# Performance work log

Measured on AMD Instinct MI355X. Metric: run time of the kernel, lower is better.

Reference implementation:

```python
import jax, jax.numpy as jnp
import numpy as np

N_NODES = 50000
N_EDGES = 600000
D_FEAT = 128
NHID = 128
N_CLASSES = 40


def gcn_conv(x, W, b, src, dst, n_nodes):
    """PyG-style GCNConv: out = D^{-1/2} (A + I) D^{-1/2} (x W) + b.

    src/dst: [E'] edge endpoints including self-loops; messages are gathered
    from src and scatter-added at dst with symmetric normalization.
    """
    h = x @ W  # [N, out] -- transform before propagate (linearity => same math)
    deg = jax.ops.segment_sum(jnp.ones_like(dst, dtype=h.dtype), dst,
                              num_segments=n_nodes)  # in-degree incl. self-loop
    dinv = jnp.where(deg > 0, jax.lax.rsqrt(deg), 0.0)
    norm = dinv[src] * dinv[dst]  # [E']
    msg = h[src] * norm[:, None]  # [E', out] gather + scale
    out = jax.ops.segment_sum(msg, dst, num_segments=n_nodes)  # scatter-add
    return out + b


def setup_inputs() -> dict:
    key = jax.random.key(0)
    ks = jax.random.split(key, 8)
    x = jax.random.normal(ks[0], (N_NODES, D_FEAT), dtype=jnp.float32)
    edge_index = jax.random.randint(ks[1], (2, N_EDGES), 0, N_NODES, dtype=jnp.int64)
    # Glorot-ish scaled params
    W1 = jax.random.normal(ks[2], (D_FEAT, NHID), dtype=jnp.float32) / np.sqrt(D_FEAT)
    b1 = jnp.zeros((NHID,), dtype=jnp.float32)
    W2 = jax.random.normal(ks[3], (NHID, NHID), dtype=jnp.float32) / np.sqrt(NHID)
    b2 = jnp.zeros((NHID,), dtype=jnp.float32)
    Wlin = jax.random.normal(ks[4], (NHID, N_CLASSES), dtype=jnp.float32) / np.sqrt(NHID)
    blin = jnp.zeros((N_CLASSES,), dtype=jnp.float32)
    return {"x": x, "edge_index": edge_index, "W1": W1, "b1": b1,
            "W2": W2, "b2": b2, "Wlin": Wlin, "blin": blin}


def reference(x, edge_index, W1, b1, W2, b2, Wlin, blin):
    n = x.shape[0]
    loop = jnp.arange(n, dtype=edge_index.dtype)
    src = jnp.concatenate([edge_index[0], loop])  # add self-loops
    dst = jnp.concatenate([edge_index[1], loop])
    h = gcn_conv(x, W1, b1, src, dst, n)
    h = jnp.tanh(h)  # dropout is identity in eval mode
    h = gcn_conv(h, W2, b2, src, dst, n)
    h = jnp.tanh(h)
    return h @ Wlin + blin  # [N, num_classes]
```

## Files before the change

### kernel.cpp

```cpp
#include <hip/hip_runtime.h>
#include <cmath>

#define D 128
#define NCLS 40
#define GG 391
#define CAP 64

typedef __bf16 bfrag __attribute__((ext_vector_type(8)));
typedef float ffrag __attribute__((ext_vector_type(4)));
typedef unsigned int u32;
typedef unsigned int u32x4 __attribute__((ext_vector_type(4)));

__device__ inline float fast_tanh(float x) {
  float ax = __builtin_fabsf(x);
  float z = __expf(-2.0f * ax);
  float r = (1.0f - z) * __builtin_amdgcn_rcpf(1.0f + z);
  return copysignf(r, x);
}

__global__ __launch_bounds__(256) void zero_deg(int* __restrict__ deg, int N) {
  int i = blockIdx.x * 256 + threadIdx.x;
  if (i < N) deg[i] = 0;
}

__global__ __launch_bounds__(256) void mega1(const float* __restrict__ A, const float* __restrict__ W1,
                                             const float* __restrict__ W2, const float* __restrict__ Wl,
                                             __bf16* __restrict__ C, int N,
                                             const int* __restrict__ src, const int* __restrict__ dst, int E,
                                             int* __restrict__ deg, int* __restrict__ csr,
                                             __bf16* __restrict__ Wt2, __bf16* __restrict__ Wlt, int EB) {
  const int b = blockIdx.x;
  const int tid = threadIdx.x;
  if (b >= GG) {
    if (b < GG + EB) {
      int e = (b - GG) * 256 + tid;
      if (e < E) {
        int s = src[e], d = dst[e];
        int pos = atomicAdd(&deg[d], 1);
        if (pos < CAP) csr[d * CAP + pos] = s;
      }
    } else {
      int j = (b - GG - EB) * 256 + tid;
      if (j < 16384) {
        Wt2[j] = (__bf16)W2[(j & 127) * D + (j >> 7)];
      } else if (j < 16384 + 48 * D) {
        int q = j - 16384;
        int n = q >> 7, k = q & 127;
        Wlt[q] = (n < NCLS) ? (__bf16)Wl[k * NCLS + n] : (__bf16)0.0f;
      }
    }
    return;
  }
  __shared__ __align__(16) __bf16 Bs[128][136];
  const int wave = tid >> 6, lane = tid & 63;
  const int row0 = b * 128 + wave * 32;
  const int koff = (lane >> 4) * 8;

  for (int i = tid; i < 128 * 128; i += 256) {
    int n = i & 127, k = i >> 7;
    Bs[n][k] = (__bf16)W1[k * D + n];
  }

  bfrag a[2][4];
#pragma unroll
  for (int mt = 0; mt < 2; ++mt) {
    int r = row0 + mt * 16 + (lane & 15);
    int rc = r < N ? r : N - 1;
    const float* p = A + (size_t)rc * D;
#pragma unroll
    for (int kk = 0; kk < 4; ++kk) {
      float4 u = *(const float4*)(p + kk * 32 + koff);
      float4 v = *(const float4*)(p + kk * 32 + koff + 4);
      bfrag f;
      f[0] = (__bf16)u.x; f[1] = (__bf16)u.y; f[2] = (__bf16)u.z; f[3] = (__bf16)u.w;
      f[4] = (__bf16)v.x; f[5] = (__bf16)v.y; f[6] = (__bf16)v.z; f[7] = (__bf16)v.w;
      a[mt][kk] = f;
    }
  }
  __syncthreads();

  ffrag acc[2][8];
#pragma unroll
  for (int mt = 0; mt < 2; ++mt)
#pragma unroll
    for (int n = 0; n < 8; ++n) acc[mt][n] = (ffrag){0.f, 0.f, 0.f, 0.f};

#pragma unroll
  for (int kk = 0; kk < 4; ++kk) {
#pragma unroll
    for (int n = 0; n < 8; ++n) {
      bfrag bb = *(const bfrag*)(&Bs[n * 16 + (lane & 15)][kk * 32 + koff]);
      acc[0][n] = __builtin_amdgcn_mfma_f32_16x16x32_bf16(a[0][kk], bb, acc[0][n], 0, 0, 0);
      acc[1][n] = __builtin_amdgcn_mfma_f32_16x16x32_bf16(a[1][kk], bb, acc[1][n], 0, 0, 0);
    }
  }

  int ocol = lane & 15;
#pragma unroll
  for (int mt = 0; mt < 2; ++mt) {
    int orow0 = row0 + mt * 16 + (lane >> 4) * 4;
#pragma unroll
    for (int n = 0; n < 8; ++n)
#pragma unroll
      for (int i = 0; i < 4; ++i) {
        int r = orow0 + i;
        if (r < N) C[(size_t)r * D + n * 16 + ocol] = (__bf16)acc[mt][n][i];
      }
  }
}

__device__ inline void gather16(const __bf16* __restrict__ t, const int* __restrict__ deg,
                                const int* __restrict__ csr, const float* __restrict__ bias,
                                __bf16 (*Hs)[136], int node0, int wave, int lane, int N) {
  const int g = lane >> 4, sl = lane & 15;
  const int node = node0 + wave * 4 + g;
  const int nd = node < N ? node : N - 1;
  const int cnt = deg[nd];
  const int jm = cnt < CAP ? cnt : CAP;
  const float dv = rsqrtf((float)cnt + 1.0f);

  int mx = jm;
  int o1 = __shfl_xor(mx, 16, 64);
  mx = mx > o1 ? mx : o1;
  int o2 = __shfl_xor(mx, 32, 64);
  mx = mx > o2 ? mx : o2;
  const int jmw = __builtin_amdgcn_readfirstlane(mx);

  bfrag tv = *(const bfrag*)(t + (size_t)nd * D + sl * 8);
  const float selfw = dv * dv;
  float acc[8];
#pragma unroll
  for (int i = 0; i < 8; ++i) acc[i] = selfw * (float)tv[i];

  for (int base = 0; base < jmw; base += 16) {
    int rem = jm - base;
    int es = nd;
    float ew = 0.0f;
    if (sl < rem) {
      es = csr[nd * CAP + base + sl];
      ew = rsqrtf((float)deg[es] + 1.0f) * dv;
    }
    int nin = jmw - base; nin = nin < 16 ? nin : 16;
    for (int j = 0; j < nin; ++j) {
      int s = __shfl(es, g * 16 + j, 64);
      float w = __shfl(ew, g * 16 + j, 64);
      bfrag r = *(const bfrag*)(t + (size_t)s * D + sl * 8);
#pragma unroll
      for (int i = 0; i < 8; ++i) acc[i] += w * (float)r[i];
    }
  }

  float4 b0 = *(const float4*)(bias + sl * 8);
  float4 b1 = *(const float4*)(bias + sl * 8 + 4);
  bfrag o;
  o[0] = (__bf16)fast_tanh(acc[0] + b0.x);
  o[1] = (__bf16)fast_tanh(acc[1] + b0.y);
  o[2] = (__bf16)fast_tanh(acc[2] + b0.z);
  o[3] = (__bf16)fast_tanh(acc[3] + b0.w);
  o[4] = (__bf16)fast_tanh(acc[4] + b1.x);
  o[5] = (__bf16)fast_tanh(acc[5] + b1.y);
  o[6] = (__bf16)fast_tanh(acc[6] + b1.z);
  o[7] = (__bf16)fast_tanh(acc[7] + b1.w);
  *(u32x4*)&Hs[wave * 4 + g][sl * 8] = *(u32x4*)&o;
}

__global__ __launch_bounds__(256) void gather_gemm(const __bf16* __restrict__ t, const int* __restrict__ deg,
                                                   const int* __restrict__ csr, const float* __restrict__ bias,
                                                   const __bf16* __restrict__ Wt, __bf16* __restrict__ C, int N) {
  __shared__ __align__(16) __bf16 Hs[16][136];
  const int tid = threadIdx.x;
  const int wave = tid >> 6, lane = tid & 63;
  const int g = lane >> 4, sl = lane & 15;
  const int node0 = blockIdx.x * 16;

  gather16(t, deg, csr, bias, Hs, node0, wave, lane, N);
  __syncthreads();

  const int koff = g * 8;
  bfrag a[4];
#pragma unroll
  for (int kk = 0; kk < 4; ++kk) a[kk] = *(const bfrag*)(&Hs[sl][kk * 32 + koff]);
  ffrag acc2[2];
  acc2[0] = (ffrag){0.f, 0.f, 0.f, 0.f};
  acc2[1] = (ffrag){0.f, 0.f, 0.f, 0.f};
#pragma unroll
  for (int nt = 0; nt < 2; ++nt) {
    const __bf16* wp = Wt + (size_t)(wave * 32 + nt * 16 + sl) * D;
    bfrag bfr[4];
#pragma unroll
    for (int kk = 0; kk < 4; ++kk) bfr[kk] = *(const bfrag*)(wp + kk * 32 + koff);
#pragma unroll
    for (int kk = 0; kk < 4; ++kk)
      acc2[nt] = __builtin_amdgcn_mfma_f32_16x16x32_bf16(a[kk], bfr[kk], acc2[nt], 0, 0, 0);
  }
#pragma unroll
  for (int nt = 0; nt < 2; ++nt) {
    int ccol = wave * 32 + nt * 16 + sl;
#pragma unroll
    for (int i = 0; i < 4; ++i) {
      int r = node0 + g * 4 + i;
      if (r < N) C[(size_t)r * D + ccol] = (__bf16)acc2[nt][i];
    }
  }
}

__global__ __launch_bounds__(256) void gather_head(const __bf16* __restrict__ t, const int* __restrict__ deg,
                                                   const int* __restrict__ csr, const float* __restrict__ bias,
                                                   const __bf16* __restrict__ Wlt, const float* __restrict__ blin,
                                                   float* __restrict__ out, int N) {
  __shared__ __align__(16) __bf16 Hs[16][136];
  const int tid = threadIdx.x;
  const int wave = tid >> 6, lane = tid & 63;
  const int g = lane >> 4, sl = lane & 15;
  const int node0 = blockIdx.x * 16;

  gather16(t, deg, csr, bias, Hs, node0, wave, lane, N);
  __syncthreads();

  if (wave < 3) {
    const int koff = g * 8;
    bfrag a[4];
#pragma unroll
    for (int kk = 0; kk < 4; ++kk) a[kk] = *(const bfrag*)(&Hs[sl][kk * 32 + koff]);
    ffrag acc2 = (ffrag){0.f, 0.f, 0.f, 0.f};
    const __bf16* wp = Wlt + (size_t)(wave * 16 + sl) * D;
    bfrag bfr[4];
#pragma unroll
    for (int kk = 0; kk < 4; ++kk) bfr[kk] = *(const bfrag*)(wp + kk * 32 + koff);
#pragma unroll
    for (int kk = 0; kk < 4; ++kk)
      acc2 = __builtin_amdgcn_mfma_f32_16x16x32_bf16(a[kk], bfr[kk], acc2, 0, 0, 0);

    int ccol = wave * 16 + sl;
    if (ccol < NCLS) {
      float bl = blin[ccol];
#pragma unroll
      for (int i = 0; i < 4; ++i) {
        int r = node0 + g * 4 + i;
        if (r < N) out[(size_t)r * NCLS + ccol] = acc2[i] + bl;
      }
    }
  }
}

extern "C" void kernel_launch(void* const* d_in, const int* in_sizes, int n_in,
                              void* d_out, int out_size, void* d_ws, size_t ws_size,
                              hipStream_t stream) {
  const float* x    = (const float*)d_in[0];
  const int*   ei   = (const int*)d_in[1];
  const float* W1   = (const float*)d_in[2];
  const float* b1   = (const float*)d_in[3];
  const float* W2   = (const float*)d_in[4];
  const float* b2   = (const float*)d_in[5];
  const float* Wlin = (const float*)d_in[6];
  const float* blin = (const float*)d_in[7];
  float* out = (float*)d_out;

  const int N = in_sizes[0] / D;
  const int E = in_sizes[1] / 2;
  const int* srcp = ei;
  const int* dstp = ei + E;

  char* ws = (char*)d_ws;
  int*    deg = (int*)ws;
  __bf16* Wt2 = (__bf16*)(ws + ((size_t)256 << 10));
  __bf16* Wlt = (__bf16*)(ws + ((size_t)320 << 10));
  int*    csr = (int*)(ws + ((size_t)1 << 20));
  __bf16* tb  = (__bf16*)(ws + ((size_t)16 << 20));
  __bf16* hb  = (__bf16*)(ws + ((size_t)32 << 20));

  const int nb = (N + 255) / 256;
  const int eb = (E + 255) / 256;
  const int cvb = (16384 + 48 * D + 255) / 256;
  const int gb = (N + 15) / 16;
  dim3 b256(256);

  zero_deg<<<nb, b256, 0, stream>>>(deg, N);
  mega1<<<GG + eb + cvb, b256, 0, stream>>>(x, W1, W2, Wlin, tb, N, srcp, dstp, E, deg, csr, Wt2, Wlt, eb);
  gather_gemm<<<gb, b256, 0, stream>>>(tb, deg, csr, b1, Wt2, hb, N);
  gather_head<<<gb, b256, 0, stream>>>(hb, deg, csr, b2, Wlt, blin, out, N);
}
```

Baseline: 188.4 us.

## Prescale node features by D^-1/2 to drop per-edge degree lookups in gathers

Factors the symmetric normalization so source rows are pre-multiplied by dinv (a new scale_rows pass for layer 1, and in the GEMM epilogue for layer 2) and the destination dinv is applied once after aggregation. This removes the per-edge deg[src] load, rsqrt and weight shuffle from the gather inner loop, which becomes a plain sum. It costs an extra kernel launch plus a full read and write of the layer-1 feature buffer, and adds rounding because the scaled values are stored in bf16.

```diff
diff --git a/kernel.cpp b/kernel.cpp
--- a/kernel.cpp
+++ b/kernel.cpp
@@ -109,15 +109,29 @@
   }
 }
 
-__device__ inline void gather16(const __bf16* __restrict__ t, const int* __restrict__ deg,
-                                const int* __restrict__ csr, const float* __restrict__ bias,
-                                __bf16 (*Hs)[136], int node0, int wave, int lane, int N) {
+__global__ __launch_bounds__(256) void scale_rows(__bf16* __restrict__ t, const int* __restrict__ deg, int N) {
+  int i = blockIdx.x * 256 + threadIdx.x;
+  int row = i >> 4;
+  if (row >= N) return;
+  float dv = rsqrtf((float)deg[row] + 1.0f);
+  __bf16* p = t + (size_t)row * D + (i & 15) * 8;
+  bfrag v = *(const bfrag*)p;
+  bfrag o;
+#pragma unroll
+  for (int k = 0; k < 8; ++k) o[k] = (__bf16)(dv * (float)v[k]);
+  *(bfrag*)p = o;
+}
+
+__device__ inline void gather16s(const __bf16* __restrict__ t, const int* __restrict__ deg,
+                                 const int* __restrict__ csr, const float* __restrict__ bias,
+                                 __bf16 (*Hs)[136], float* dvs, int node0, int wave, int lane, int N) {
   const int g = lane >> 4, sl = lane & 15;
   const int node = node0 + wave * 4 + g;
   const int nd = node < N ? node : N - 1;
   const int cnt = deg[nd];
   const int jm = cnt < CAP ? cnt : CAP;
   const float dv = rsqrtf((float)cnt + 1.0f);
+  if (sl == 0) dvs[wave * 4 + g] = dv;
 
   int mx = jm;
   int o1 = __shfl_xor(mx, 16, 64);
@@ -127,40 +141,36 @@
   const int jmw = __builtin_amdgcn_readfirstlane(mx);
 
   bfrag tv = *(const bfrag*)(t + (size_t)nd * D + sl * 8);
-  const float selfw = dv * dv;
   float acc[8];
 #pragma unroll
-  for (int i = 0; i < 8; ++i) acc[i] = selfw * (float)tv[i];
+  for (int i = 0; i < 8; ++i) acc[i] = (float)tv[i];
 
   for (int base = 0; base < jmw; base += 16) {
     int rem = jm - base;
     int es = nd;
-    float ew = 0.0f;
-    if (sl < rem) {
-      es = csr[nd * CAP + base + sl];
-      ew = rsqrtf((float)deg[es] + 1.0f) * dv;
-    }
+    if (sl < rem) es = csr[nd * CAP + base + sl];
     int nin = jmw - base; nin = nin < 16 ? nin : 16;
     for (int j = 0; j < nin; ++j) {
       int s = __shfl(es, g * 16 + j, 64);
-      float w = __shfl(ew, g * 16 + j, 64);
       bfrag r = *(const bfrag*)(t + (size_t)s * D + sl * 8);
-#pragma unroll
-      for (int i = 0; i < 8; ++i) acc[i] += w * (float)r[i];
+      if (base + j < jm) {
+#pragma unroll
+        for (int i = 0; i < 8; ++i) acc[i] += (float)r[i];
+      }
     }
   }
 
   float4 b0 = *(const float4*)(bias + sl * 8);
   float4 b1 = *(const float4*)(bias + sl * 8 + 4);
   bfrag o;
-  o[0] = (__bf16)fast_tanh(acc[0] + b0.x);
-  o[1] = (__bf16)fast_tanh(acc[1] + b0.y);
-  o[2] = (__bf16)fast_tanh(acc[2] + b0.z);
-  o[3] = (__bf16)fast_tanh(acc[3] + b0.w);
-  o[4] = (__bf16)fast_tanh(acc[4] + b1.x);
-  o[5] = (__bf16)fast_tanh(acc[5] + b1.y);
-  o[6] = (__bf16)fast_tanh(acc[6] + b1.z);
-  o[7] = (__bf16)fast_tanh(acc[7] + b1.w);
+  o[0] = (__bf16)fast_tanh(dv * acc[0] + b0.x);
+  o[1] = (__bf16)fast_tanh(dv * acc[1] + b0.y);
+  o[2] = (__bf16)fast_tanh(dv * acc[2] + b0.z);
+  o[3] = (__bf16)fast_tanh(dv * acc[3] + b0.w);
+  o[4] = (__bf16)fast_tanh(dv * acc[4] + b1.x);
+  o[5] = (__bf16)fast_tanh(dv * acc[5] + b1.y);
+  o[6] = (__bf16)fast_tanh(dv * acc[6] + b1.z);
+  o[7] = (__bf16)fast_tanh(dv * acc[7] + b1.w);
   *(u32x4*)&Hs[wave * 4 + g][sl * 8] = *(u32x4*)&o;
 }
 
@@ -168,12 +178,13 @@
                                                    const int* __restrict__ csr, const float* __restrict__ bias,
                                                    const __bf16* __restrict__ Wt, __bf16* __restrict__ C, int N) {
   __shared__ __align__(16) __bf16 Hs[16][136];
+  __shared__ float dvs[16];
   const int tid = threadIdx.x;
   const int wave = tid >> 6, lane = tid & 63;
   const int g = lane >> 4, sl = lane & 15;
   const int node0 = blockIdx.x * 16;
 
-  gather16(t, deg, csr, bias, Hs, node0, wave, lane, N);
+  gather16s(t, deg, csr, bias, Hs, dvs, node0, wave, lane, N);
   __syncthreads();
 
   const int koff = g * 8;
@@ -199,7 +210,7 @@
 #pragma unroll
     for (int i = 0; i < 4; ++i) {
       int r = node0 + g * 4 + i;
-      if (r < N) C[(size_t)r * D + ccol] = (__bf16)acc2[nt][i];
+      if (r < N) C[(size_t)r * D + ccol] = (__bf16)(dvs[g * 4 + i] * acc2[nt][i]);
     }
   }
 }
@@ -209,12 +220,13 @@
                                                    const __bf16* __restrict__ Wlt, const float* __restrict__ blin,
                                                    float* __restrict__ out, int N) {
   __shared__ __align__(16) __bf16 Hs[16][136];
+  __shared__ float dvs[16];
   const int tid = threadIdx.x;
   const int wave = tid >> 6, lane = tid & 63;
   const int g = lane >> 4, sl = lane & 15;
   const int node0 = blockIdx.x * 16;
 
-  gather16(t, deg, csr, bias, Hs, node0, wave, lane, N);
+  gather16s(t, deg, csr, bias, Hs, dvs, node0, wave, lane, N);
   __syncthreads();
 
   if (wave < 3) {
@@ -277,6 +289,7 @@
 
   zero_deg<<<nb, b256, 0, stream>>>(deg, N);
   mega1<<<GG + eb + cvb, b256, 0, stream>>>(x, W1, W2, Wlin, tb, N, srcp, dstp, E, deg, csr, Wt2, Wlt, eb);
+  scale_rows<<<(N * 16 + 255) / 256, b256, 0, stream>>>(tb, deg, N);
   gather_gemm<<<gb, b256, 0, stream>>>(tb, deg, csr, b1, Wt2, hb, N);
   gather_head<<<gb, b256, 0, stream>>>(hb, deg, csr, b2, Wlt, blin, out, N);
 }
```

Result: no change. 185.3 us (-1.6%).
